# Optimization experiments

Hardware: AMD Instinct MI355X
Metric: run time of the kernel (lower is better)

The kernel has to match this reference:

```python
import jax, jax.numpy as jnp
import numpy as np

BIG = 1e30  # stands in for sys.maxsize in fp32-safe form


def _find_neg_anchors(e_actv, host):
    # Full pairwise Euclidean distance matrix (equivalent to the
    # pdist -> triangular reconstruction in the torch code).
    sq = jnp.sum(e_actv * e_actv, axis=1)                       # [n]
    d2 = sq[:, None] + sq[None, :] - 2.0 * (e_actv @ e_actv.T)  # [n, n]
    dist = jnp.sqrt(jnp.maximum(d2, 0.0))
    n = e_actv.shape[0]
    # mask: self (diagonal) and same-discriminator pairs -> huge distance
    same_discr = host[:, None] == host[None, :]
    eye = jnp.eye(n, dtype=bool)
    dist = jnp.where(same_discr | eye, BIG, dist)
    idxs = jnp.argmin(dist, axis=1)                             # [n]
    return e_actv[idxs]                                         # gather


def setup_inputs() -> dict:
    key = jax.random.key(0)
    k1, k2, k3 = jax.random.split(key, 3)
    n, d = 8192, 256
    e_actv = jax.random.normal(k1, (n, d), dtype=jnp.float32)
    e_ap = jax.random.normal(k2, (n, d), dtype=jnp.float32)
    host = jax.random.randint(k3, (n,), 0, 64, dtype=jnp.int64 if jax.config.read('jax_enable_x64') else jnp.int32)
    return {"e_actv": e_actv, "e_ap": e_ap, "host": host}


def reference(e_actv, e_ap, host):
    # forward returns (e_actv, e_ap, e_an); e_an computed under no_grad
    e_an = jax.lax.stop_gradient(_find_neg_anchors(e_actv, host))
    return (e_actv, e_ap, e_an)
```

## Files before the change

### kernel.cpp

```cpp
#include <hip/hip_runtime.h>
#include <hip/hip_bf16.h>
#include <cmath>
#include <cstddef>

#define N 8192
#define D 256
#define BI 128
#define KT 32
#define NT (N / BI)
#define NTRI (NT * (NT + 1) / 2)

typedef __attribute__((ext_vector_type(8))) short short8;
typedef __attribute__((ext_vector_type(4))) float float4v;

__device__ inline ushort f2bf(float x) {
    __hip_bfloat16 h = __float2bfloat16(x);
    return __builtin_bit_cast(ushort, h);
}
__device__ inline float bf2f(ushort u) {
    __hip_bfloat16 h = __builtin_bit_cast(__hip_bfloat16, u);
    return __bfloat162float(h);
}

__device__ inline void gl_lds16(const void* g, void* l) {
    __builtin_amdgcn_global_load_lds(
        (const __attribute__((address_space(1))) void*)g,
        (__attribute__((address_space(3))) void*)l,
        16, 0, 0);
}

__device__ inline unsigned long long packKI(float k, int idx) {
    unsigned u = __float_as_uint(k);
    u = (u & 0x80000000u) ? ~u : (u | 0x80000000u);
    return ((unsigned long long)u << 32) | (unsigned)idx;
}

__device__ inline int triT(int t) { return t * (129 - t) / 2; }

__global__ void prep_kernel(const float4* __restrict__ a, const float4* __restrict__ p,
                            float4* __restrict__ out, float* __restrict__ sq,
                            ushort4* __restrict__ hi, ushort4* __restrict__ lo,
                            unsigned long long* __restrict__ M) {
    const int gsz = gridDim.x * blockDim.x;
    const int g0 = blockIdx.x * blockDim.x + threadIdx.x;
    const int total = N * D / 4;

    for (int idx = g0; idx < total; idx += gsz) {
        float4 v = a[idx];
        out[idx] = v;
        ushort4 h, l;
        h.x = f2bf(v.x); l.x = f2bf(v.x - bf2f(h.x));
        h.y = f2bf(v.y); l.y = f2bf(v.y - bf2f(h.y));
        h.z = f2bf(v.z); l.z = f2bf(v.z - bf2f(h.z));
        h.w = f2bf(v.w); l.w = f2bf(v.w - bf2f(h.w));
        hi[idx] = h; lo[idx] = l;
        float s = v.x * v.x + v.y * v.y + v.z * v.z + v.w * v.w;
        #pragma unroll
        for (int off = 32; off; off >>= 1) s += __shfl_down(s, off);
        if ((threadIdx.x & 63) == 0) sq[idx >> 6] = s;
    }
    for (int idx = g0; idx < total; idx += gsz) out[total + idx] = p[idx];
    for (int i = g0; i < N; i += gsz) M[i] = 0xFFFFFFFFFFFFFFFFull;
}

__launch_bounds__(256)
__global__ void argmin_sym(const ushort* __restrict__ Ehi, const ushort* __restrict__ Elo,
                           const int* __restrict__ host, const float* __restrict__ sq,
                           unsigned long long* __restrict__ M) {
    const int b = blockIdx.x;
    int ti = (int)floor(64.5 - sqrt(64.5 * 64.5 - 2.0 * (double)b));
    while (triT(ti + 1) <= b) ti++;
    while (triT(ti) > b) ti--;
    const int tj = ti + (b - triT(ti));

    __shared__ __align__(16) ushort lds[4 * BI * KT];
    __shared__ float sqA_s[BI], sqB_s[BI];
    __shared__ int   hostB_s[BI];
    ushort* Ahi_s = lds;
    ushort* Alo_s = lds + 1 * BI * KT;
    ushort* Bhi_s = lds + 2 * BI * KT;
    ushort* Blo_s = lds + 3 * BI * KT;

    const int ib0 = ti * BI;
    const int jb0 = tj * BI;
    const int tid = threadIdx.x;
    const int lane = tid & 63;
    const int wave = tid >> 6;
    const int wrow = wave >> 1;
    const int wcol = wave & 1;
    const int tx = lane & 15;
    const int q  = lane >> 4;

    unsigned hostAp[4];
    #pragma unroll
    for (int rt = 0; rt < 4; rt++) {
        unsigned p = 0;
        #pragma unroll
        for (int reg = 0; reg < 4; reg++) {
            int hv = host[ib0 + wrow * 64 + rt * 16 + q * 4 + reg];
            p |= ((unsigned)hv & 0xFFu) << (8 * reg);
        }
        hostAp[rt] = p;
    }

    float4v acc[4][4];
    #pragma unroll
    for (int rt = 0; rt < 4; rt++)
        #pragma unroll
        for (int ct = 0; ct < 4; ct++) acc[rt][ct] = (float4v)(0.0f);

    for (int kt = 0; kt < D; kt += KT) {
        __syncthreads();
        #pragma unroll
        for (int t = 0; t < 2; t++) {
            int f = tid + t * 256;
            int row = f >> 2;
            int c = f & 3;
            size_t gA = (size_t)(ib0 + row) * D + kt + c * 8;
            size_t gB = (size_t)(jb0 + row) * D + kt + c * 8;
            int o = f * 8;
            gl_lds16(&Ehi[gA], &Ahi_s[o]);
            gl_lds16(&Elo[gA], &Alo_s[o]);
            gl_lds16(&Ehi[gB], &Bhi_s[o]);
            gl_lds16(&Elo[gB], &Blo_s[o]);
        }
        if (kt == 0 && tid < BI) {
            sqA_s[tid] = sq[ib0 + tid];
            sqB_s[tid] = sq[jb0 + tid];
            hostB_s[tid] = host[jb0 + tid];
        }
        __syncthreads();

        short8 ah[4], al[4], bh[4], bl[4];
        #pragma unroll
        for (int rt = 0; rt < 4; rt++) {
            int o = (wrow * 64 + rt * 16 + tx) * KT + q * 8;
            ah[rt] = *(const short8*)&Ahi_s[o];
            al[rt] = *(const short8*)&Alo_s[o];
        }
        #pragma unroll
        for (int ct = 0; ct < 4; ct++) {
            int o = (wcol * 64 + ct * 16 + tx) * KT + q * 8;
            bh[ct] = *(const short8*)&Bhi_s[o];
            bl[ct] = *(const short8*)&Blo_s[o];
        }
        #pragma unroll
        for (int rt = 0; rt < 4; rt++)
            #pragma unroll
            for (int ct = 0; ct < 4; ct++)
                acc[rt][ct] = __builtin_amdgcn_mfma_f32_16x16x32_bf16(ah[rt], bh[ct], acc[rt][ct], 0, 0, 0);
        #pragma unroll
        for (int rt = 0; rt < 4; rt++)
            #pragma unroll
            for (int ct = 0; ct < 4; ct++)
                acc[rt][ct] = __builtin_amdgcn_mfma_f32_16x16x32_bf16(ah[rt], bl[ct], acc[rt][ct], 0, 0, 0);
        #pragma unroll
        for (int rt = 0; rt < 4; rt++)
            #pragma unroll
            for (int ct = 0; ct < 4; ct++)
                acc[rt][ct] = __builtin_amdgcn_mfma_f32_16x16x32_bf16(al[rt], bh[ct], acc[rt][ct], 0, 0, 0);
    }

    __syncthreads();
    float* rowV = (float*)lds;
    int*   rowI = (int*)lds + 256;
    float* colV = (float*)lds + 512;
    int*   colI = (int*)lds + 768;

    #pragma unroll
    for (int rt = 0; rt < 4; rt++) {
        unsigned hp = hostAp[rt];
        #pragma unroll
        for (int reg = 0; reg < 4; reg++) {
            int il = wrow * 64 + rt * 16 + q * 4 + reg;
            int ig = ib0 + il;
            int ha = (int)((hp >> (8 * reg)) & 0xFFu);
            float v = 3.0e38f; int ix = 0x7fffffff;
            #pragma unroll
            for (int ct = 0; ct < 4; ct++) {
                int jl = wcol * 64 + ct * 16 + tx;
                int jg = jb0 + jl;
                float key = sqB_s[jl] - 2.0f * acc[rt][ct][reg];
                bool masked = (hostB_s[jl] == ha) || (jg == ig);
                if (!masked && (key < v || (key == v && jg < ix))) { v = key; ix = jg; }
            }
            #pragma unroll
            for (int d = 1; d < 16; d <<= 1) {
                float ov = __shfl_xor(v, d);
                int   oi = __shfl_xor(ix, d);
                if (ov < v || (ov == v && oi < ix)) { v = ov; ix = oi; }
            }
            if (tx == 0) { rowV[il * 2 + wcol] = v; rowI[il * 2 + wcol] = ix; }
        }
    }

    if (ti != tj) {
        #pragma unroll
        for (int ct = 0; ct < 4; ct++) {
            int jl = wcol * 64 + ct * 16 + tx;
            int hb = hostB_s[jl];
            float v = 3.0e38f; int ix = 0x7fffffff;
            #pragma unroll
            for (int rt = 0; rt < 4; rt++) {
                unsigned hp = hostAp[rt];
                #pragma unroll
                for (int reg = 0; reg < 4; reg++) {
                    int il = wrow * 64 + rt * 16 + q * 4 + reg;
                    int ig = ib0 + il;
                    bool masked = ((int)((hp >> (8 * reg)) & 0xFFu) == hb);
                    float key = sqA_s[il] - 2.0f * acc[rt][ct][reg];
                    if (!masked && (key < v || (key == v && ig < ix))) { v = key; ix = ig; }
                }
            }
            #pragma unroll
            for (int d = 16; d < 64; d <<= 1) {
                float ov = __shfl_xor(v, d);
                int   oi = __shfl_xor(ix, d);
                if (ov < v || (ov == v && oi < ix)) { v = ov; ix = oi; }
            }
            if (q == 0) { colV[jl * 2 + wrow] = v; colI[jl * 2 + wrow] = ix; }
        }
    }

    __syncthreads();
    if (tid < BI) {
        float v0 = rowV[tid * 2];     int x0 = rowI[tid * 2];
        float v1 = rowV[tid * 2 + 1]; int x1 = rowI[tid * 2 + 1];
        if (v1 < v0 || (v1 == v0 && x1 < x0)) { v0 = v1; x0 = x1; }
        atomicMin(&M[ib0 + tid], packKI(v0, x0));
        if (ti != tj) {
            float w0 = colV[tid * 2];     int y0 = colI[tid * 2];
            float w1 = colV[tid * 2 + 1]; int y1 = colI[tid * 2 + 1];
            if (w1 < w0 || (w1 == w0 && y1 < y0)) { w0 = w1; y0 = y1; }
            atomicMin(&M[jb0 + tid], packKI(w0, y0));
        }
    }
}

__global__ void finalize_kernel(const unsigned long long* __restrict__ M,
                                const float* __restrict__ E, float* __restrict__ out_an) {
    int row = blockIdx.x;
    int t = threadIdx.x;
    int idx = (int)(unsigned)(M[row] & 0xFFFFFFFFull);
    float4 v = *(const float4*)&E[(size_t)idx * D + t * 4];
    *(float4*)&out_an[(size_t)row * D + t * 4] = v;
}

extern "C" void kernel_launch(void* const* d_in, const int* in_sizes, int n_in,
                              void* d_out, int out_size, void* d_ws, size_t ws_size,
                              hipStream_t stream) {
    const float* e_actv = (const float*)d_in[0];
    const float* e_ap   = (const float*)d_in[1];
    const int*   host   = (const int*)d_in[2];
    float* out = (float*)d_out;

    unsigned long long* M = (unsigned long long*)d_ws;
    float*  sq  = (float*)(M + N);
    ushort* Ehi = (ushort*)(sq + N);
    ushort* Elo = Ehi + (size_t)N * D;

    prep_kernel<<<1024, 256, 0, stream>>>(
        (const float4*)e_actv, (const float4*)e_ap, (float4*)out,
        sq, (ushort4*)Ehi, (ushort4*)Elo, M);
    argmin_sym<<<NTRI, 256, 0, stream>>>(Ehi, Elo, host, sq, M);
    finalize_kernel<<<N, 64, 0, stream>>>(M, e_actv, out + 2 * (size_t)N * D);
}
```

Before: 204.2 us.

## Double-buffer LDS tiles to overlap global loads with MFMA compute

Doubles the LDS staging buffer and prefetches the next K-slice via global_load_lds while the current slice is consumed by MFMAs, using explicit vmcnt waits and raw barriers instead of two __syncthreads per iteration. The goal is to hide global memory latency in the symmetric Gram/argmin kernel. It doubles LDS usage (to about 64KB), which may reduce occupancy, and relies on hand-tuned waitcnt counts being correct.

New measurement: 196.6 us. -3.8%, faster.

```diff
diff --git a/kernel.cpp b/kernel.cpp
--- a/kernel.cpp
+++ b/kernel.cpp
@@ -9,6 +9,7 @@
 #define KT 32
 #define NT (N / BI)
 #define NTRI (NT * (NT + 1) / 2)
+#define BUFSZ (4 * BI * KT)
 
 typedef __attribute__((ext_vector_type(8))) short short8;
 typedef __attribute__((ext_vector_type(4))) float float4v;
@@ -73,13 +74,9 @@
     while (triT(ti) > b) ti--;
     const int tj = ti + (b - triT(ti));
 
-    __shared__ __align__(16) ushort lds[4 * BI * KT];
+    __shared__ __align__(16) ushort lds[2 * BUFSZ];
     __shared__ float sqA_s[BI], sqB_s[BI];
     __shared__ int   hostB_s[BI];
-    ushort* Ahi_s = lds;
-    ushort* Alo_s = lds + 1 * BI * KT;
-    ushort* Bhi_s = lds + 2 * BI * KT;
-    ushort* Blo_s = lds + 3 * BI * KT;
 
     const int ib0 = ti * BI;
     const int jb0 = tj * BI;
@@ -109,27 +106,45 @@
         #pragma unroll
         for (int ct = 0; ct < 4; ct++) acc[rt][ct] = (float4v)(0.0f);
 
-    for (int kt = 0; kt < D; kt += KT) {
-        __syncthreads();
+    if (tid < BI) {
+        sqA_s[tid] = sq[ib0 + tid];
+        sqB_s[tid] = sq[jb0 + tid];
+        hostB_s[tid] = host[jb0 + tid];
+    }
+
+    auto STAGE = [&](int s, int kk) {
+        ushort* base = lds + s * BUFSZ;
         #pragma unroll
         for (int t = 0; t < 2; t++) {
             int f = tid + t * 256;
             int row = f >> 2;
             int c = f & 3;
-            size_t gA = (size_t)(ib0 + row) * D + kt + c * 8;
-            size_t gB = (size_t)(jb0 + row) * D + kt + c * 8;
+            size_t gA = (size_t)(ib0 + row) * D + kk + c * 8;
+            size_t gB = (size_t)(jb0 + row) * D + kk + c * 8;
             int o = f * 8;
-            gl_lds16(&Ehi[gA], &Ahi_s[o]);
-            gl_lds16(&Elo[gA], &Alo_s[o]);
-            gl_lds16(&Ehi[gB], &Bhi_s[o]);
-            gl_lds16(&Elo[gB], &Blo_s[o]);
-        }
-        if (kt == 0 && tid < BI) {
-            sqA_s[tid] = sq[ib0 + tid];
-            sqB_s[tid] = sq[jb0 + tid];
-            hostB_s[tid] = host[jb0 + tid];
-        }
-        __syncthreads();
+            gl_lds16(&Ehi[gA], &base[o]);
+            gl_lds16(&Elo[gA], &base[1 * BI * KT + o]);
+            gl_lds16(&Ehi[gB], &base[2 * BI * KT + o]);
+            gl_lds16(&Elo[gB], &base[3 * BI * KT + o]);
+        }
+    };
+
+    STAGE(0, 0);
+
+    for (int kt = 0; kt < D; kt += KT) {
+        const int cur = (kt >> 5) & 1;
+        if (kt + KT < D) {
+            STAGE(cur ^ 1, kt + KT);
+            asm volatile("s_waitcnt vmcnt(8)" ::: "memory");
+        } else {
+            asm volatile("s_waitcnt vmcnt(0)" ::: "memory");
+        }
+        __builtin_amdgcn_s_barrier();
+
+        const ushort* Ahi_s = lds + cur * BUFSZ;
+        const ushort* Alo_s = Ahi_s + 1 * BI * KT;
+        const ushort* Bhi_s = Ahi_s + 2 * BI * KT;
+        const ushort* Blo_s = Ahi_s + 3 * BI * KT;
 
         short8 ah[4], al[4], bh[4], bl[4];
         #pragma unroll
@@ -159,6 +174,9 @@
             #pragma unroll
             for (int ct = 0; ct < 4; ct++)
                 acc[rt][ct] = __builtin_amdgcn_mfma_f32_16x16x32_bf16(al[rt], bh[ct], acc[rt][ct], 0, 0, 0);
+
+        asm volatile("s_waitcnt lgkmcnt(0)" ::: "memory");
+        __builtin_amdgcn_s_barrier();
     }
 
     __syncthreads();
```

## Pre-swizzle bf16 split operands into MFMA fragment layout and load directly from global

Applied to the files above, without the earlier changes.

The prep kernel now writes the hi/lo bf16 split of the activations in a per-16-row, per-k-chunk fragment layout that matches the MFMA operand order. The argmin kernel then reads operands straight from global memory (via cache) into registers instead of staging them through LDS with per-chunk barriers. It also adds an occupancy hint of two blocks per SM and remaps block indices across the triangle to spread tiles. This removes LDS traffic and syncs but relies on L1/L2 to serve the repeated tile reads, which may raise global load latency.

After: 185.3 us. -9.3%, faster.

```diff
diff --git a/kernel.cpp b/kernel.cpp
--- a/kernel.cpp
+++ b/kernel.cpp
@@ -6,7 +6,6 @@
 #define N 8192
 #define D 256
 #define BI 128
-#define KT 32
 #define NT (N / BI)
 #define NTRI (NT * (NT + 1) / 2)
 
@@ -20,13 +19,6 @@
 __device__ inline float bf2f(ushort u) {
     __hip_bfloat16 h = __builtin_bit_cast(__hip_bfloat16, u);
     return __bfloat162float(h);
-}
-
-__device__ inline void gl_lds16(const void* g, void* l) {
-    __builtin_amdgcn_global_load_lds(
-        (const __attribute__((address_space(1))) void*)g,
-        (__attribute__((address_space(3))) void*)l,
-        16, 0, 0);
 }
 
 __device__ inline unsigned long long packKI(float k, int idx) {
@@ -37,9 +29,10 @@
 
 __device__ inline int triT(int t) { return t * (129 - t) / 2; }
 
+
 __global__ void prep_kernel(const float4* __restrict__ a, const float4* __restrict__ p,
                             float4* __restrict__ out, float* __restrict__ sq,
-                            ushort4* __restrict__ hi, ushort4* __restrict__ lo,
+                            ushort* __restrict__ Ehi, ushort* __restrict__ Elo,
                             unsigned long long* __restrict__ M) {
     const int gsz = gridDim.x * blockDim.x;
     const int g0 = blockIdx.x * blockDim.x + threadIdx.x;
@@ -48,38 +41,56 @@
     for (int idx = g0; idx < total; idx += gsz) {
         float4 v = a[idx];
         out[idx] = v;
-        ushort4 h, l;
-        h.x = f2bf(v.x); l.x = f2bf(v.x - bf2f(h.x));
-        h.y = f2bf(v.y); l.y = f2bf(v.y - bf2f(h.y));
-        h.z = f2bf(v.z); l.z = f2bf(v.z - bf2f(h.z));
-        h.w = f2bf(v.w); l.w = f2bf(v.w - bf2f(h.w));
-        hi[idx] = h; lo[idx] = l;
         float s = v.x * v.x + v.y * v.y + v.z * v.z + v.w * v.w;
         #pragma unroll
         for (int off = 32; off; off >>= 1) s += __shfl_down(s, off);
         if ((threadIdx.x & 63) == 0) sq[idx >> 6] = s;
     }
     for (int idx = g0; idx < total; idx += gsz) out[total + idx] = p[idx];
+
+    {
+        const int w = g0 >> 6;
+        if (w < 4096) {
+            const int lane = threadIdx.x & 63;
+            const int tx = lane & 15;
+            const int q  = lane >> 4;
+            const int r16 = w >> 3;
+            const int ktc = w & 7;
+            const int row = r16 * 16 + tx;
+            const float4 v0 = a[row * 64 + ktc * 8 + q * 2];
+            const float4 v1 = a[row * 64 + ktc * 8 + q * 2 + 1];
+            float e[8] = {v0.x, v0.y, v0.z, v0.w, v1.x, v1.y, v1.z, v1.w};
+            short8 hs, ls;
+            #pragma unroll
+            for (int j = 0; j < 8; j++) {
+                ushort h = f2bf(e[j]);
+                ushort l = f2bf(e[j] - bf2f(h));
+                hs[j] = (short)h;
+                ls[j] = (short)l;
+            }
+            const size_t off = (size_t)(r16 * 8 + ktc) * 512 + lane * 8;
+            *(short8*)&Ehi[off] = hs;
+            *(short8*)&Elo[off] = ls;
+        }
+    }
     for (int i = g0; i < N; i += gsz) M[i] = 0xFFFFFFFFFFFFFFFFull;
 }
 
-__launch_bounds__(256)
+__launch_bounds__(256, 2)
 __global__ void argmin_sym(const ushort* __restrict__ Ehi, const ushort* __restrict__ Elo,
                            const int* __restrict__ host, const float* __restrict__ sq,
                            unsigned long long* __restrict__ M) {
-    const int b = blockIdx.x;
+    const int b0 = blockIdx.x;
+    const int b = (b0 & 7) * (NTRI / 8) + (b0 >> 3);
     int ti = (int)floor(64.5 - sqrt(64.5 * 64.5 - 2.0 * (double)b));
     while (triT(ti + 1) <= b) ti++;
     while (triT(ti) > b) ti--;
     const int tj = ti + (b - triT(ti));
 
-    __shared__ __align__(16) ushort lds[4 * BI * KT];
     __shared__ float sqA_s[BI], sqB_s[BI];
     __shared__ int   hostB_s[BI];
-    ushort* Ahi_s = lds;
-    ushort* Alo_s = lds + 1 * BI * KT;
-    ushort* Bhi_s = lds + 2 * BI * KT;
-    ushort* Blo_s = lds + 3 * BI * KT;
+    __shared__ float rowV[2 * BI]; __shared__ int rowI[2 * BI];
+    __shared__ float colV[2 * BI]; __shared__ int colI[2 * BI];
 
     const int ib0 = ti * BI;
     const int jb0 = tj * BI;
@@ -91,6 +102,12 @@
     const int tx = lane & 15;
     const int q  = lane >> 4;
 
+    if (tid < BI) {
+        sqA_s[tid] = sq[ib0 + tid];
+        sqB_s[tid] = sq[jb0 + tid];
+        hostB_s[tid] = host[jb0 + tid];
+    }
+
     unsigned hostAp[4];
     #pragma unroll
     for (int rt = 0; rt < 4; rt++) {
@@ -109,40 +126,24 @@
         #pragma unroll
         for (int ct = 0; ct < 4; ct++) acc[rt][ct] = (float4v)(0.0f);
 
-    for (int kt = 0; kt < D; kt += KT) {
-        __syncthreads();
-        #pragma unroll
-        for (int t = 0; t < 2; t++) {
-            int f = tid + t * 256;
-            int row = f >> 2;
-            int c = f & 3;
-            size_t gA = (size_t)(ib0 + row) * D + kt + c * 8;
-            size_t gB = (size_t)(jb0 + row) * D + kt + c * 8;
-            int o = f * 8;
-            gl_lds16(&Ehi[gA], &Ahi_s[o]);
-            gl_lds16(&Elo[gA], &Alo_s[o]);
-            gl_lds16(&Ehi[gB], &Bhi_s[o]);
-            gl_lds16(&Elo[gB], &Blo_s[o]);
-        }
-        if (kt == 0 && tid < BI) {
-            sqA_s[tid] = sq[ib0 + tid];
-            sqB_s[tid] = sq[jb0 + tid];
-            hostB_s[tid] = host[jb0 + tid];
-        }
-        __syncthreads();
-
+    const int pA = (ib0 >> 4) + wrow * 4;
+    const int pB = (jb0 >> 4) + wcol * 4;
+    const int lo8 = lane * 8;
+
+    #pragma unroll
+    for (int ktc = 0; ktc < 8; ktc++) {
         short8 ah[4], al[4], bh[4], bl[4];
         #pragma unroll
         for (int rt = 0; rt < 4; rt++) {
-            int o = (wrow * 64 + rt * 16 + tx) * KT + q * 8;
-            ah[rt] = *(const short8*)&Ahi_s[o];
-            al[rt] = *(const short8*)&Alo_s[o];
+            const int o = ((pA + rt) * 8 + ktc) * 512 + lo8;
+            ah[rt] = *(const short8*)&Ehi[o];
+            al[rt] = *(const short8*)&Elo[o];
         }
         #pragma unroll
         for (int ct = 0; ct < 4; ct++) {
-            int o = (wcol * 64 + ct * 16 + tx) * KT + q * 8;
-            bh[ct] = *(const short8*)&Bhi_s[o];
-            bl[ct] = *(const short8*)&Blo_s[o];
+            const int o = ((pB + ct) * 8 + ktc) * 512 + lo8;
+            bh[ct] = *(const short8*)&Ehi[o];
+            bl[ct] = *(const short8*)&Elo[o];
         }
         #pragma unroll
         for (int rt = 0; rt < 4; rt++)
@@ -162,10 +163,6 @@
     }
 
     __syncthreads();
-    float* rowV = (float*)lds;
-    int*   rowI = (int*)lds + 256;
-    float* colV = (float*)lds + 512;
-    int*   colI = (int*)lds + 768;
 
     #pragma unroll
     for (int rt = 0; rt < 4; rt++) {
@@ -261,7 +258,7 @@
 
     prep_kernel<<<1024, 256, 0, stream>>>(
         (const float4*)e_actv, (const float4*)e_ap, (float4*)out,
-        sq, (ushort4*)Ehi, (ushort4*)Elo, M);
+        sq, Ehi, Elo, M);
     argmin_sym<<<NTRI, 256, 0, stream>>>(Ehi, Elo, host, sq, M);
     finalize_kernel<<<N, 64, 0, stream>>>(M, e_actv, out + 2 * (size_t)N * D);
 }
```
